# Kernel tuning notes

Hardware: AMD Instinct MI355X
Metric: run time of the kernel (lower is better)

## Reference

```python
import jax, jax.numpy as jnp
import numpy as np

BATCH, LENGTH, FEAT, RANK = 4096, 128, 4, 64
SCALE = 1.0 / np.sqrt(RANK)  # keep 128-step matrix chain numerically stable


def setup_inputs() -> dict:
    key = jax.random.key(0)
    k1, k2, k3, k4 = jax.random.split(key, 4)
    return {
        "input_data": jax.random.normal(k1, (BATCH, LENGTH, FEAT), dtype=jnp.float32),
        "first_core": jax.random.normal(k2, (FEAT, RANK), dtype=jnp.float32) * SCALE,
        "mid_cores": jax.random.normal(k3, (LENGTH - 2, RANK, FEAT, RANK), dtype=jnp.float32) * SCALE,
        "last_core": jax.random.normal(k4, (RANK, FEAT), dtype=jnp.float32) * SCALE,
    }


def reference(input_data, first_core, mid_cores, last_core):
    # input_data: [b, L, f] -> site-major [L, b, f]
    x = jnp.transpose(input_data, (1, 0, 2))
    # Per-site contraction with the physical (feature) index.
    v0 = jnp.einsum("ir,bi->br", first_core, x[0])            # [b, r]
    mid_mats = jnp.einsum("slir,sbi->sblr", mid_cores, x[1:-1])  # [S, b, r, r]
    last_vec = jnp.einsum("li,bi->bl", last_core, x[-1])      # [b, r]

    # Sequential tensor-train chain: v <- v @ M_s for each middle site.
    def step(v, mat):
        return jnp.einsum("bl,blr->br", v, mat), None

    v, _ = jax.lax.scan(step, v0, mid_mats)
    # Final contraction against last site vector -> [b, 1]
    out = jnp.sum(v * last_vec, axis=-1, keepdims=True)
    return out
```

## Files before the change

kernel.cpp:

```cpp
#include <hip/hip_runtime.h>
#include <stdint.h>

#define NSITES 126
#define XPITCH 516
#define VPH    72

typedef _Float16 half8_t  __attribute__((ext_vector_type(8)));
typedef float    float4_t __attribute__((ext_vector_type(4)));

#define LBAR() asm volatile("s_waitcnt lgkmcnt(0)\n\ts_barrier" ::: "memory")
#define WAITV(N) asm volatile("s_waitcnt vmcnt(" #N ")" ::: "memory")
#define TIE8(F) asm volatile("" : "+v"(F[0]), "+v"(F[1]), "+v"(F[2]), "+v"(F[3]), \
                                  "+v"(F[4]), "+v"(F[5]), "+v"(F[6]), "+v"(F[7]))

__device__ __forceinline__ void aload(half8_t& d, const void* p) {
    asm volatile("global_load_dwordx4 %0, %1, off" : "=v"(d) : "v"(p));
}

__global__ __launch_bounds__(256) void repack_g(const float* __restrict__ mid,
                                                _Float16* __restrict__ gt) {
    const int F = blockIdx.x * 256 + threadIdx.x;
    const int lane = F & 63, w = (F >> 6) & 3, h = (F >> 8) & 1, i = (F >> 9) & 3;
    const int s = F >> 11;
    const int q = lane >> 4, c = lane & 15;
    const float* src = mid + (size_t)s * 16384 + (32 * h + 8 * q) * 256 + i * 64 + w * 16 + c;
    half8_t o;
#pragma unroll
    for (int j = 0; j < 8; ++j) o[j] = (_Float16)src[j * 256];
    ((half8_t*)gt)[F] = o;
}

__global__ __launch_bounds__(256) void tt_chain(
    const float* __restrict__ x,
    const float* __restrict__ first,
    const float* __restrict__ last,
    const _Float16* __restrict__ gt,
    float* __restrict__ out) {

    __shared__ __align__(16) _Float16 vbuf[2][16 * VPH];
    __shared__ float xbuf[16 * XPITCH];
    __shared__ int   eacc[16];

    const int tid  = threadIdx.x;
    const int w    = tid >> 6;
    const int lane = tid & 63;
    const int q    = lane >> 4;
    const int c    = lane & 15;
    const int b0   = blockIdx.x * 16;

    {
        const int bb = tid >> 4, seg = tid & 15;
        const float4_t* src = (const float4_t*)(x + (size_t)(b0 + bb) * 512 + seg * 32);
        float4_t* dst = (float4_t*)(xbuf + bb * XPITCH + seg * 32);
#pragma unroll
        for (int k = 0; k < 8; ++k) dst[k] = src[k];
    }
    if (tid < 16) eacc[tid] = 0;
    __syncthreads();

    {
        const int bb = tid >> 4, rq = tid & 15;
        const float xs0 = xbuf[bb * XPITCH + 0], xs1 = xbuf[bb * XPITCH + 1];
        const float xs2 = xbuf[bb * XPITCH + 2], xs3 = xbuf[bb * XPITCH + 3];
#pragma unroll
        for (int k = 0; k < 4; ++k) {
            const int r = rq * 4 + k;
            vbuf[0][bb * VPH + r] = (_Float16)(
                xs0 * first[r] + xs1 * first[64 + r] + xs2 * first[128 + r] + xs3 * first[192 + r]);
        }
    }

    half8_t F0[8], F1[8], F2[8];
    const char* gbase = (const char*)gt + w * 1024 + lane * 16;
    auto LOAD = [&](int s, half8_t* F) {
        const char* p = gbase + (size_t)s * 32768;
#pragma unroll
        for (int ih = 0; ih < 8; ++ih) aload(F[ih], p + ih * 4096);
    };
    LOAD(0, F0);
    LOAD(1, F1);
    LBAR();

    auto STEP = [&](int s, half8_t* F) {
        const int p = s & 1;

        const _Float16* vr = &vbuf[p][c * VPH];
        half8_t af0 = *(const half8_t*)(vr + q * 8);
        half8_t af1 = *(const half8_t*)(vr + 32 + q * 8);
        float4_t xs[4];
#pragma unroll
        for (int jj = 0; jj < 4; ++jj)
            xs[jj] = *(const float4_t*)(xbuf + (q * 4 + jj) * XPITCH + (s + 1) * 4);

        WAITV(16);
        TIE8(F);

        if ((s & 7) == 0 && s != 0) {
            float a[16];
#pragma unroll
            for (int k = 0; k < 8; ++k) { a[k] = (float)af0[k]; a[8 + k] = (float)af1[k]; }
            float m = 0.f;
#pragma unroll
            for (int k = 0; k < 16; ++k) m = fmaxf(m, fabsf(a[k]));
            m = fmaxf(m, __shfl_xor(m, 16));
            m = fmaxf(m, __shfl_xor(m, 32));
            int e = 0;
            if (m > 0.f) frexpf(m, &e);
            const float sc = ldexpf(1.0f, -e);
#pragma unroll
            for (int k = 0; k < 8; ++k) {
                af0[k] = (_Float16)(a[k] * sc);
                af1[k] = (_Float16)(a[8 + k] * sc);
            }
            if (tid < 16) eacc[tid] += e;
        }

        float4_t acc[4];
#pragma unroll
        for (int i = 0; i < 4; ++i) {
            float4_t z = {0.f, 0.f, 0.f, 0.f};
            z = __builtin_amdgcn_mfma_f32_16x16x32_f16(af0, F[i * 2 + 0], z, 0, 0, 0);
            z = __builtin_amdgcn_mfma_f32_16x16x32_f16(af1, F[i * 2 + 1], z, 0, 0, 0);
            acc[i] = z;
        }

#pragma unroll
        for (int jj = 0; jj < 4; ++jj) {
            const float vn = xs[jj].x * acc[0][jj] + xs[jj].y * acc[1][jj] +
                             xs[jj].z * acc[2][jj] + xs[jj].w * acc[3][jj];
            vbuf[p ^ 1][(q * 4 + jj) * VPH + w * 16 + c] = (_Float16)vn;
        }
        LBAR();
    };

    for (int s = 0; s < NSITES; s += 3) {
        const int s2 = (s + 2 < NSITES) ? s + 2 : NSITES - 1;
        const int s3 = (s + 3 < NSITES) ? s + 3 : NSITES - 1;
        const int s4 = (s + 4 < NSITES) ? s + 4 : NSITES - 1;
        LOAD(s2, F2);
        STEP(s, F0);
        LOAD(s3, F0);
        STEP(s + 1, F1);
        LOAD(s4, F1);
        STEP(s + 2, F2);
    }
    WAITV(0);

    {
        const int bb = tid >> 4, rq = tid & 15;
        const float x0 = xbuf[bb * XPITCH + 508], x1 = xbuf[bb * XPITCH + 509];
        const float x2 = xbuf[bb * XPITCH + 510], x3 = xbuf[bb * XPITCH + 511];
        float dot = 0.f;
#pragma unroll
        for (int k = 0; k < 4; ++k) {
            const int r = rq * 4 + k;
            const float lv = last[r * 4 + 0] * x0 + last[r * 4 + 1] * x1 +
                             last[r * 4 + 2] * x2 + last[r * 4 + 3] * x3;
            dot += lv * (float)vbuf[0][bb * VPH + r];
        }
#pragma unroll
        for (int o = 8; o > 0; o >>= 1) dot += __shfl_xor(dot, o, 16);
        if (rq == 0) out[b0 + bb] = ldexpf(dot, eacc[bb]);
    }
}

extern "C" void kernel_launch(void* const* d_in, const int* in_sizes, int n_in,
                              void* d_out, int out_size, void* d_ws, size_t ws_size,
                              hipStream_t stream) {
    (void)in_sizes; (void)n_in; (void)out_size; (void)ws_size;
    const float* x     = (const float*)d_in[0];
    const float* first = (const float*)d_in[1];
    const float* mid   = (const float*)d_in[2];
    const float* last  = (const float*)d_in[3];
    float* out = (float*)d_out;
    _Float16* gt = (_Float16*)d_ws;

    repack_g<<<1008, 256, 0, stream>>>(mid, gt);
    tt_chain<<<256, 256, 0, stream>>>(x, first, last, gt, out);
}
```

Measured before the change: 120.8 us.

## Fuse weight repack into chain kernel with a grid-wide software barrier

Merges the separate fp16 repack kernel into the main chain kernel. Each of the 256 blocks repacks a strided slice of the middle cores, then all blocks meet at a global atomic-counter barrier before the chain starts. This removes one kernel launch and the gap between the two kernels. In exchange, all 256 blocks must be co-resident for the spin barrier to finish, and only 256 blocks now do the repack instead of 1008.

```diff
diff --git a/kernel.cpp b/kernel.cpp
--- a/kernel.cpp
+++ b/kernel.cpp
@@ -17,24 +17,14 @@
     asm volatile("global_load_dwordx4 %0, %1, off" : "=v"(d) : "v"(p));
 }
 
-__global__ __launch_bounds__(256) void repack_g(const float* __restrict__ mid,
-                                                _Float16* __restrict__ gt) {
-    const int F = blockIdx.x * 256 + threadIdx.x;
-    const int lane = F & 63, w = (F >> 6) & 3, h = (F >> 8) & 1, i = (F >> 9) & 3;
-    const int s = F >> 11;
-    const int q = lane >> 4, c = lane & 15;
-    const float* src = mid + (size_t)s * 16384 + (32 * h + 8 * q) * 256 + i * 64 + w * 16 + c;
-    half8_t o;
-#pragma unroll
-    for (int j = 0; j < 8; ++j) o[j] = (_Float16)src[j * 256];
-    ((half8_t*)gt)[F] = o;
-}
+__device__ unsigned long long g_bar;
 
-__global__ __launch_bounds__(256) void tt_chain(
+__global__ __launch_bounds__(256) void fused(
     const float* __restrict__ x,
     const float* __restrict__ first,
     const float* __restrict__ last,
-    const _Float16* __restrict__ gt,
+    const float* __restrict__ mid,
+    _Float16* __restrict__ gt,
     float* __restrict__ out) {
 
     __shared__ __align__(16) _Float16 vbuf[2][16 * VPH];
@@ -47,6 +37,17 @@
     const int q    = lane >> 4;
     const int c    = lane & 15;
     const int b0   = blockIdx.x * 16;
+
+    for (int F = blockIdx.x * 256 + tid; F < NSITES * 2048; F += 256 * 256) {
+        const int fl = F & 63, fw = (F >> 6) & 3, fh = (F >> 8) & 1, fi = (F >> 9) & 3;
+        const int fs = F >> 11;
+        const int fq = fl >> 4, fc = fl & 15;
+        const float* src = mid + (size_t)fs * 16384 + (32 * fh + 8 * fq) * 256 + fi * 64 + fw * 16 + fc;
+        half8_t o;
+#pragma unroll
+        for (int j = 0; j < 8; ++j) o[j] = (_Float16)src[j * 256];
+        ((half8_t*)gt)[F] = o;
+    }
 
     {
         const int bb = tid >> 4, seg = tid & 15;
@@ -69,6 +70,17 @@
                 xs0 * first[r] + xs1 * first[64 + r] + xs2 * first[128 + r] + xs3 * first[192 + r]);
         }
     }
+
+    __syncthreads();
+    if (tid == 0) {
+        __threadfence();
+        const unsigned long long my = atomicAdd(&g_bar, 1ull);
+        const unsigned long long target = (my / 256 + 1) * 256;
+        while (__hip_atomic_load(&g_bar, __ATOMIC_ACQUIRE, __HIP_MEMORY_SCOPE_AGENT) < target)
+            __builtin_amdgcn_s_sleep(8);
+        __threadfence();
+    }
+    __syncthreads();
 
     half8_t F0[8], F1[8], F2[8];
     const char* gbase = (const char*)gt + w * 1024 + lane * 16;
@@ -175,6 +187,5 @@
     float* out = (float*)d_out;
     _Float16* gt = (_Float16*)d_ws;
 
-    repack_g<<<1008, 256, 0, stream>>>(mid, gt);
-    tt_chain<<<256, 256, 0, stream>>>(x, first, last, gt, out);
+    fused<<<256, 256, 0, stream>>>(x, first, last, mid, gt, out);
 }
```

Result: slower. 139.7 us (+15.7%).

## Split K-dimension of chain step across two wave groups with fp32 partial sums

Applied to the files above, without the earlier changes.

Doubles the block to 512 threads and splits the rank-64 contraction into two halves, each handled by four waves issuing one MFMA per feature instead of two. Partial products are stored in fp32 LDS buffers and summed by the consumer on the next step. The renormalisation max is now computed one step ahead from the summed fp32 values, which avoids a shuffle reduction on the critical path. The aim is to shorten per-step latency on the serial chain, at the cost of extra LDS traffic and a larger block, with the 256 blocks still at one block per CU.

```diff
diff --git a/kernel.cpp b/kernel.cpp
--- a/kernel.cpp
+++ b/kernel.cpp
@@ -3,15 +3,14 @@
 
 #define NSITES 126
 #define XPITCH 516
-#define VPH    72
+#define VPF    68
 
 typedef _Float16 half8_t  __attribute__((ext_vector_type(8)));
 typedef float    float4_t __attribute__((ext_vector_type(4)));
 
 #define LBAR() asm volatile("s_waitcnt lgkmcnt(0)\n\ts_barrier" ::: "memory")
 #define WAITV(N) asm volatile("s_waitcnt vmcnt(" #N ")" ::: "memory")
-#define TIE8(F) asm volatile("" : "+v"(F[0]), "+v"(F[1]), "+v"(F[2]), "+v"(F[3]), \
-                                  "+v"(F[4]), "+v"(F[5]), "+v"(F[6]), "+v"(F[7]))
+#define TIE4(F) asm volatile("" : "+v"(F[0]), "+v"(F[1]), "+v"(F[2]), "+v"(F[3]))
 
 __device__ __forceinline__ void aload(half8_t& d, const void* p) {
     asm volatile("global_load_dwordx4 %0, %1, off" : "=v"(d) : "v"(p));
@@ -30,52 +29,56 @@
     ((half8_t*)gt)[F] = o;
 }
 
-__global__ __launch_bounds__(256) void tt_chain(
+__global__ __launch_bounds__(512, 1) void tt_chain(
     const float* __restrict__ x,
     const float* __restrict__ first,
     const float* __restrict__ last,
     const _Float16* __restrict__ gt,
     float* __restrict__ out) {
 
-    __shared__ __align__(16) _Float16 vbuf[2][16 * VPH];
     __shared__ float xbuf[16 * XPITCH];
+    __shared__ __align__(16) float pbuf[2][2][16 * VPF];
+    __shared__ float hmf[2][16];
     __shared__ int   eacc[16];
 
     const int tid  = threadIdx.x;
     const int w    = tid >> 6;
+    const int wv   = w & 3;
+    const int h    = w >> 2;
     const int lane = tid & 63;
     const int q    = lane >> 4;
     const int c    = lane & 15;
     const int b0   = blockIdx.x * 16;
 
     {
-        const int bb = tid >> 4, seg = tid & 15;
-        const float4_t* src = (const float4_t*)(x + (size_t)(b0 + bb) * 512 + seg * 32);
-        float4_t* dst = (float4_t*)(xbuf + bb * XPITCH + seg * 32);
+        const int bb = tid >> 5, seg = tid & 31;
+        const float4_t* src = (const float4_t*)(x + (size_t)(b0 + bb) * 512);
+        float4_t* dst = (float4_t*)(xbuf + bb * XPITCH);
 #pragma unroll
-        for (int k = 0; k < 8; ++k) dst[k] = src[k];
+        for (int k = 0; k < 4; ++k) dst[seg + 32 * k] = src[seg + 32 * k];
     }
     if (tid < 16) eacc[tid] = 0;
     __syncthreads();
 
-    {
+    if (tid < 256) {
         const int bb = tid >> 4, rq = tid & 15;
         const float xs0 = xbuf[bb * XPITCH + 0], xs1 = xbuf[bb * XPITCH + 1];
         const float xs2 = xbuf[bb * XPITCH + 2], xs3 = xbuf[bb * XPITCH + 3];
 #pragma unroll
         for (int k = 0; k < 4; ++k) {
             const int r = rq * 4 + k;
-            vbuf[0][bb * VPH + r] = (_Float16)(
-                xs0 * first[r] + xs1 * first[64 + r] + xs2 * first[128 + r] + xs3 * first[192 + r]);
+            pbuf[0][0][bb * VPF + r] =
+                xs0 * first[r] + xs1 * first[64 + r] + xs2 * first[128 + r] + xs3 * first[192 + r];
+            pbuf[0][1][bb * VPF + r] = 0.f;
         }
     }
 
-    half8_t F0[8], F1[8], F2[8];
-    const char* gbase = (const char*)gt + w * 1024 + lane * 16;
+    half8_t F0[4], F1[4], F2[4];
+    const char* gbase = (const char*)gt + h * 4096 + wv * 1024 + lane * 16;
     auto LOAD = [&](int s, half8_t* F) {
         const char* p = gbase + (size_t)s * 32768;
 #pragma unroll
-        for (int ih = 0; ih < 8; ++ih) aload(F[ih], p + ih * 4096);
+        for (int f = 0; f < 4; ++f) aload(F[f], p + f * 8192);
     };
     LOAD(0, F0);
     LOAD(1, F1);
@@ -84,51 +87,54 @@
     auto STEP = [&](int s, half8_t* F) {
         const int p = s & 1;
 
-        const _Float16* vr = &vbuf[p][c * VPH];
-        half8_t af0 = *(const half8_t*)(vr + q * 8);
-        half8_t af1 = *(const half8_t*)(vr + 32 + q * 8);
+        const float* r0 = &pbuf[p][0][c * VPF + 32 * h + 8 * q];
+        const float* r1 = &pbuf[p][1][c * VPF + 32 * h + 8 * q];
+        float4_t alo = *(const float4_t*)r0 + *(const float4_t*)r1;
+        float4_t ahi = *(const float4_t*)(r0 + 4) + *(const float4_t*)(r1 + 4);
         float4_t xs[4];
 #pragma unroll
         for (int jj = 0; jj < 4; ++jj)
             xs[jj] = *(const float4_t*)(xbuf + (q * 4 + jj) * XPITCH + (s + 1) * 4);
 
-        WAITV(16);
-        TIE8(F);
-
         if ((s & 7) == 0 && s != 0) {
-            float a[16];
-#pragma unroll
-            for (int k = 0; k < 8; ++k) { a[k] = (float)af0[k]; a[8 + k] = (float)af1[k]; }
-            float m = 0.f;
-#pragma unroll
-            for (int k = 0; k < 16; ++k) m = fmaxf(m, fabsf(a[k]));
-            m = fmaxf(m, __shfl_xor(m, 16));
-            m = fmaxf(m, __shfl_xor(m, 32));
+            const float mx = 2.0f * fmaxf(hmf[0][c], hmf[1][c]);
             int e = 0;
-            if (m > 0.f) frexpf(m, &e);
+            if (mx > 0.f) frexpf(mx, &e);
             const float sc = ldexpf(1.0f, -e);
 #pragma unroll
-            for (int k = 0; k < 8; ++k) {
-                af0[k] = (_Float16)(a[k] * sc);
-                af1[k] = (_Float16)(a[8 + k] * sc);
-            }
-            if (tid < 16) eacc[tid] += e;
+            for (int k = 0; k < 4; ++k) { alo[k] *= sc; ahi[k] *= sc; }
+            if (w == 0 && lane < 16) eacc[lane] += e;
         }
+        if ((s & 7) == 7 && s < 120) {
+            float hl = 0.f;
+#pragma unroll
+            for (int k = 0; k < 4; ++k)
+                hl = fmaxf(hl, fmaxf(fabsf(alo[k]), fabsf(ahi[k])));
+            hl = fmaxf(hl, __shfl_xor(hl, 16));
+            hl = fmaxf(hl, __shfl_xor(hl, 32));
+            if (wv == 0 && q == 0) hmf[h][c] = hl;
+        }
+
+        half8_t af;
+#pragma unroll
+        for (int k = 0; k < 4; ++k) { af[k] = (_Float16)alo[k]; af[4 + k] = (_Float16)ahi[k]; }
+
+        WAITV(8);
+        TIE4(F);
 
         float4_t acc[4];
 #pragma unroll
-        for (int i = 0; i < 4; ++i) {
+        for (int f = 0; f < 4; ++f) {
             float4_t z = {0.f, 0.f, 0.f, 0.f};
-            z = __builtin_amdgcn_mfma_f32_16x16x32_f16(af0, F[i * 2 + 0], z, 0, 0, 0);
-            z = __builtin_amdgcn_mfma_f32_16x16x32_f16(af1, F[i * 2 + 1], z, 0, 0, 0);
-            acc[i] = z;
+            acc[f] = __builtin_amdgcn_mfma_f32_16x16x32_f16(af, F[f], z, 0, 0, 0);
         }
 
+        float* pw = &pbuf[p ^ 1][h][0];
 #pragma unroll
         for (int jj = 0; jj < 4; ++jj) {
-            const float vn = xs[jj].x * acc[0][jj] + xs[jj].y * acc[1][jj] +
-                             xs[jj].z * acc[2][jj] + xs[jj].w * acc[3][jj];
-            vbuf[p ^ 1][(q * 4 + jj) * VPH + w * 16 + c] = (_Float16)vn;
+            const float vn = xs[jj][0] * acc[0][jj] + xs[jj][1] * acc[1][jj] +
+                             xs[jj][2] * acc[2][jj] + xs[jj][3] * acc[3][jj];
+            pw[(q * 4 + jj) * VPF + wv * 16 + c] = vn;
         }
         LBAR();
     };
@@ -146,7 +152,7 @@
     }
     WAITV(0);
 
-    {
+    if (tid < 256) {
         const int bb = tid >> 4, rq = tid & 15;
         const float x0 = xbuf[bb * XPITCH + 508], x1 = xbuf[bb * XPITCH + 509];
         const float x2 = xbuf[bb * XPITCH + 510], x3 = xbuf[bb * XPITCH + 511];
@@ -156,7 +162,8 @@
             const int r = rq * 4 + k;
             const float lv = last[r * 4 + 0] * x0 + last[r * 4 + 1] * x1 +
                              last[r * 4 + 2] * x2 + last[r * 4 + 3] * x3;
-            dot += lv * (float)vbuf[0][bb * VPH + r];
+            const float v = pbuf[0][0][bb * VPF + r] + pbuf[0][1][bb * VPF + r];
+            dot += lv * v;
         }
 #pragma unroll
         for (int o = 8; o > 0; o >>= 1) dot += __shfl_xor(dot, o, 16);
@@ -176,5 +183,5 @@
     _Float16* gt = (_Float16*)d_ws;
 
     repack_g<<<1008, 256, 0, stream>>>(mid, gt);
-    tt_chain<<<256, 256, 0, stream>>>(x, first, last, gt, out);
+    tt_chain<<<256, 512, 0, stream>>>(x, first, last, gt, out);
 }
```

New measurement: 127.8 us. 1.06x slower.

## Split chain into two alternating wave teams for compute/load ping-pong

Applied to the files above, without the earlier changes.

Doubles the block to 512 threads, split into two teams of four waves. The teams alternate sites: one runs the MFMA step while the other issues global loads for future sites and prefetches x values into registers, separated by barriers. The aim is to hide the load latency and the LDS reads of x behind the other team's compute, keeping each team's register footprint lower. In exchange it adds a barrier per site, leaves half the waves idle at any moment, and relies on a fragile vmcnt wait count that must stay correct under the new per-team load schedule.

```diff
diff --git a/kernel.cpp b/kernel.cpp
--- a/kernel.cpp
+++ b/kernel.cpp
@@ -30,7 +30,7 @@
     ((half8_t*)gt)[F] = o;
 }
 
-__global__ __launch_bounds__(256) void tt_chain(
+__global__ __launch_bounds__(512, 2) void tt_chain(
     const float* __restrict__ x,
     const float* __restrict__ first,
     const float* __restrict__ last,
@@ -43,22 +43,24 @@
 
     const int tid  = threadIdx.x;
     const int w    = tid >> 6;
+    const int team = w >> 2;
+    const int wv   = w & 3;
     const int lane = tid & 63;
     const int q    = lane >> 4;
     const int c    = lane & 15;
     const int b0   = blockIdx.x * 16;
 
     {
-        const int bb = tid >> 4, seg = tid & 15;
-        const float4_t* src = (const float4_t*)(x + (size_t)(b0 + bb) * 512 + seg * 32);
-        float4_t* dst = (float4_t*)(xbuf + bb * XPITCH + seg * 32);
+        const int bb = tid >> 5, seg = tid & 31;
+        const float4_t* src = (const float4_t*)(x + (size_t)(b0 + bb) * 512);
+        float4_t* dst = (float4_t*)(xbuf + bb * XPITCH);
 #pragma unroll
-        for (int k = 0; k < 8; ++k) dst[k] = src[k];
+        for (int k = 0; k < 4; ++k) dst[seg + 32 * k] = src[seg + 32 * k];
     }
     if (tid < 16) eacc[tid] = 0;
     __syncthreads();
 
-    {
+    if (tid < 256) {
         const int bb = tid >> 4, rq = tid & 15;
         const float xs0 = xbuf[bb * XPITCH + 0], xs1 = xbuf[bb * XPITCH + 1];
         const float xs2 = xbuf[bb * XPITCH + 2], xs3 = xbuf[bb * XPITCH + 3];
@@ -71,26 +73,29 @@
     }
 
     half8_t F0[8], F1[8], F2[8];
-    const char* gbase = (const char*)gt + w * 1024 + lane * 16;
+    const char* gbase = (const char*)gt + wv * 1024 + lane * 16;
     auto LOAD = [&](int s, half8_t* F) {
         const char* p = gbase + (size_t)s * 32768;
 #pragma unroll
         for (int ih = 0; ih < 8; ++ih) aload(F[ih], p + ih * 4096);
     };
-    LOAD(0, F0);
-    LOAD(1, F1);
+
+    float4_t xs[4];
+    auto XRD = [&](int s) {
+#pragma unroll
+        for (int jj = 0; jj < 4; ++jj)
+            xs[jj] = *(const float4_t*)(xbuf + (q * 4 + jj) * XPITCH + (s + 1) * 4);
+    };
+
+    if (team == 0) { LOAD(0, F0); LOAD(2, F1); LOAD(4, F2); XRD(0); }
+    else           { LOAD(1, F0); LOAD(3, F1); }
     LBAR();
 
     auto STEP = [&](int s, half8_t* F) {
         const int p = s & 1;
-
         const _Float16* vr = &vbuf[p][c * VPH];
         half8_t af0 = *(const half8_t*)(vr + q * 8);
         half8_t af1 = *(const half8_t*)(vr + 32 + q * 8);
-        float4_t xs[4];
-#pragma unroll
-        for (int jj = 0; jj < 4; ++jj)
-            xs[jj] = *(const float4_t*)(xbuf + (q * 4 + jj) * XPITCH + (s + 1) * 4);
 
         WAITV(16);
         TIE8(F);
@@ -128,25 +133,33 @@
         for (int jj = 0; jj < 4; ++jj) {
             const float vn = xs[jj].x * acc[0][jj] + xs[jj].y * acc[1][jj] +
                              xs[jj].z * acc[2][jj] + xs[jj].w * acc[3][jj];
-            vbuf[p ^ 1][(q * 4 + jj) * VPH + w * 16 + c] = (_Float16)vn;
+            vbuf[p ^ 1][(q * 4 + jj) * VPH + wv * 16 + c] = (_Float16)vn;
         }
-        LBAR();
     };
 
-    for (int s = 0; s < NSITES; s += 3) {
-        const int s2 = (s + 2 < NSITES) ? s + 2 : NSITES - 1;
-        const int s3 = (s + 3 < NSITES) ? s + 3 : NSITES - 1;
-        const int s4 = (s + 4 < NSITES) ? s + 4 : NSITES - 1;
-        LOAD(s2, F2);
-        STEP(s, F0);
-        LOAD(s3, F0);
-        STEP(s + 1, F1);
-        LOAD(s4, F1);
-        STEP(s + 2, F2);
+    for (int B = 0; B < NSITES; B += 6) {
+        if (team == 0) STEP(B + 0, F0);
+        else { LOAD((B + 5 < NSITES) ? B + 5 : 125, F2); XRD(B + 1); }
+        LBAR();
+        if (team == 1) STEP(B + 1, F0);
+        else { LOAD((B + 6 < NSITES) ? B + 6 : 124, F0); XRD(B + 2); }
+        LBAR();
+        if (team == 0) STEP(B + 2, F1);
+        else { LOAD((B + 7 < NSITES) ? B + 7 : 125, F0); XRD(B + 3); }
+        LBAR();
+        if (team == 1) STEP(B + 3, F1);
+        else { LOAD((B + 8 < NSITES) ? B + 8 : 124, F1); XRD(B + 4); }
+        LBAR();
+        if (team == 0) STEP(B + 4, F2);
+        else { LOAD((B + 9 < NSITES) ? B + 9 : 125, F1); XRD(B + 5); }
+        LBAR();
+        if (team == 1) STEP(B + 5, F2);
+        else { LOAD((B + 10 < NSITES) ? B + 10 : 124, F2); XRD(B + 6); }
+        LBAR();
     }
     WAITV(0);
 
-    {
+    if (tid < 256) {
         const int bb = tid >> 4, rq = tid & 15;
         const float x0 = xbuf[bb * XPITCH + 508], x1 = xbuf[bb * XPITCH + 509];
         const float x2 = xbuf[bb * XPITCH + 510], x3 = xbuf[bb * XPITCH + 511];
@@ -176,5 +189,5 @@
     _Float16* gt = (_Float16*)d_ws;
 
     repack_g<<<1008, 256, 0, stream>>>(mid, gt);
-    tt_chain<<<256, 256, 0, stream>>>(x, first, last, gt, out);
+    tt_chain<<<256, 512, 0, stream>>>(x, first, last, gt, out);
 }
```

Result: faster. 111.0 us (median of 2 runs) (-8.1%).
